# Kernel tuning notes

Hardware: AMD Instinct MI355X
Metric: run time of the kernel (lower is better)

## Reference

```python
import jax, jax.numpy as jnp
import numpy as np

N, D_FEAT, D, H, L = 2048, 128, 256, 8, 2
DH = D // H
E = 65536
NUM_EDGE_TYPES = 8
MAX_DIST = 10
MAX_DEGREE = 512
D_FF = 4 * D
D_OUT = 128
EPS = 1e-5


def _layernorm(x, g, b):
    mu = jnp.mean(x, axis=-1, keepdims=True)
    var = jnp.mean(jnp.square(x - mu), axis=-1, keepdims=True)
    return (x - mu) * jax.lax.rsqrt(var + EPS) * g + b


def setup_inputs() -> dict:
    key = jax.random.key(0)
    ks = jax.random.split(key, 32)
    inp = {
        "x": jax.random.normal(ks[0], (N, D_FEAT), dtype=jnp.float32),
        "edge_index": jax.random.randint(ks[1], (2, E), 0, N),
        "edge_types": jax.random.randint(ks[2], (E,), 0, NUM_EDGE_TYPES),
        "pos_encoding": jax.random.uniform(ks[3], (N, N), dtype=jnp.float32),
    }
    def xavier(k, shape):
        fan_in, fan_out = shape[0], shape[1]
        lim = float(np.sqrt(6.0 / (fan_in + fan_out)))
        return jax.random.uniform(k, shape, jnp.float32, -lim, lim)
    inp["W_emb"] = xavier(ks[4], (D_FEAT, D)); inp["b_emb"] = jnp.zeros((D,), jnp.float32)
    # stacked per-layer params, stored as [in, out] so y = x @ W + b
    inp["Wq"] = jnp.stack([xavier(jax.random.fold_in(ks[5], l), (D, D)) for l in range(L)])
    inp["Wk"] = jnp.stack([xavier(jax.random.fold_in(ks[6], l), (D, D)) for l in range(L)])
    inp["Wv"] = jnp.stack([xavier(jax.random.fold_in(ks[7], l), (D, D)) for l in range(L)])
    inp["Wo"] = jnp.stack([xavier(jax.random.fold_in(ks[8], l), (D, D)) for l in range(L)])
    for nm in ("bq", "bk", "bv", "bo"):
        inp[nm] = jnp.zeros((L, D), jnp.float32)
    inp["spd_table"] = 0.02 * jax.random.normal(ks[9], (L, MAX_DIST + 1, H), dtype=jnp.float32)
    inp["edge_table"] = 0.02 * jax.random.normal(ks[10], (L, NUM_EDGE_TYPES, H), dtype=jnp.float32)
    inp["din_emb"] = 0.02 * jax.random.normal(ks[11], (L, MAX_DEGREE + 1, D), dtype=jnp.float32)
    inp["dout_emb"] = 0.02 * jax.random.normal(ks[12], (L, MAX_DEGREE + 1, D), dtype=jnp.float32)
    inp["ln1_g"] = jnp.ones((L, D), jnp.float32); inp["ln1_b"] = jnp.zeros((L, D), jnp.float32)
    inp["ln2_g"] = jnp.ones((L, D), jnp.float32); inp["ln2_b"] = jnp.zeros((L, D), jnp.float32)
    inp["W1"] = jnp.stack([xavier(jax.random.fold_in(ks[13], l), (D, D_FF)) for l in range(L)])
    inp["b1"] = jnp.zeros((L, D_FF), jnp.float32)
    inp["W2"] = jnp.stack([xavier(jax.random.fold_in(ks[14], l), (D_FF, D)) for l in range(L)])
    inp["b2"] = jnp.zeros((L, D), jnp.float32)
    inp["W_out"] = xavier(ks[15], (D, D_OUT)); inp["b_out"] = jnp.zeros((D_OUT,), jnp.float32)
    return inp


def _forward(x, edge_index, edge_types, pos_encoding,
             W_emb, b_emb, Wq, bq, Wk, bk, Wv, bv, Wo, bo,
             spd_table, edge_table, din_emb, dout_emb,
             ln1_g, ln1_b, ln2_g, ln2_b, W1, b1, W2, b2, W_out, b_out):
    src, dst = edge_index[0], edge_index[1]
    ones = jnp.ones((E,), jnp.int32)
    deg_out = jnp.clip(jax.ops.segment_sum(ones, src, num_segments=N), 0, MAX_DEGREE)
    deg_in = jnp.clip(jax.ops.segment_sum(ones, dst, num_segments=N), 0, MAX_DEGREE)
    # SPD bucket matrix [N, N] (int), shared across layers
    spd_bucket = jnp.clip(pos_encoding[:, :N] * MAX_DIST + 0.5, 0, MAX_DIST).astype(jnp.int32)

    h = x @ W_emb + b_emb  # node embedding; dropout=0 (eval)
    scale = 1.0 / np.sqrt(DH)
    for l in range(L):
        # centrality encoding
        h = h + din_emb[l][deg_in] + dout_emb[l][deg_out]
        xn = _layernorm(h, ln1_g[l], ln1_b[l])
        q = (xn @ Wq[l] + bq[l]).reshape(N, H, DH).transpose(1, 0, 2)  # [H,N,DH]
        k = (xn @ Wk[l] + bk[l]).reshape(N, H, DH).transpose(1, 0, 2)
        v = (xn @ Wv[l] + bv[l]).reshape(N, H, DH).transpose(1, 0, 2)
        # attention bias [H, N, N]: SPD table gather + per-edge scatter-add
        bias = spd_table[l][spd_bucket].transpose(2, 0, 1)
        e_bias = edge_table[l][edge_types]  # [E, H]
        bias = bias.at[:, src, dst].add(e_bias.T)
        scores = jnp.einsum('hnd,hmd->hnm', q, k) * scale + bias
        attn = jax.nn.softmax(scores, axis=-1)
        attn_out = jnp.einsum('hnm,hmd->hnd', attn, v).transpose(1, 0, 2).reshape(N, D)
        h = h + attn_out @ Wo[l] + bo[l]
        y = _layernorm(h, ln2_g[l], ln2_b[l])
        y = jax.nn.gelu(y @ W1[l] + b1[l], approximate=False) @ W2[l] + b2[l]
        h = h + y
    return h @ W_out + b_out


def reference(x, edge_index, edge_types, pos_encoding,
              W_emb, b_emb, Wq, bq, Wk, bk, Wv, bv, Wo, bo,
              spd_table, edge_table, din_emb, dout_emb,
              ln1_g, ln1_b, ln2_g, ln2_b, W1, b1, W2, b2, W_out, b_out):
    return _forward(x, edge_index, edge_types, pos_encoding,
                    W_emb, b_emb, Wq, bq, Wk, bk, Wv, bv, Wo, bo,
                    spd_table, edge_table, din_emb, dout_emb,
                    ln1_g, ln1_b, ln2_g, ln2_b, W1, b1, W2, b2, W_out, b_out)
```

## Files before the change

### kernel.cpp

```cpp
#include <hip/hip_runtime.h>
#include <math.h>

#define N_NODES 2048
#define D_MODEL 256
#define D_FEAT 128
#define NHEAD 8
#define DH 32
#define NLAYER 2
#define NEDGE 65536
#define D_FF 1024
#define D_OUT 128
#define MAXDEG 512
#define JSPLIT 4

typedef __attribute__((ext_vector_type(8))) short short8;
typedef __attribute__((ext_vector_type(4))) float f32x4;
typedef __attribute__((ext_vector_type(4))) unsigned short u16x4;

__device__ __forceinline__ unsigned short f2bf(float f) {
    unsigned u = __float_as_uint(f);
    unsigned r = (u + 0x7FFFu + ((u >> 16) & 1u)) >> 16;
    return (unsigned short)r;
}

__global__ void degree_kernel(const int* __restrict__ edge_index,
                              int* __restrict__ deg_out, int* __restrict__ deg_in) {
    int e = blockIdx.x * 256 + threadIdx.x;
    if (e < NEDGE) {
        atomicAdd(&deg_out[edge_index[e]], 1);
        atomicAdd(&deg_in[edge_index[NEDGE + e]], 1);
    }
}

__global__ void centrality_kernel(float* __restrict__ h,
                                  const float* __restrict__ din_l,
                                  const float* __restrict__ dout_l,
                                  const int* __restrict__ deg_in,
                                  const int* __restrict__ deg_out) {
    int idx = blockIdx.x * 256 + threadIdx.x;
    int row = idx >> 8;
    int c = idx & 255;
    int di = min(deg_in[row], MAXDEG);
    int dn = min(deg_out[row], MAXDEG);
    h[idx] += din_l[di * D_MODEL + c] + dout_l[dn * D_MODEL + c];
}

__global__ void layernorm_kernel(const float* __restrict__ x,
                                 const float* __restrict__ g,
                                 const float* __restrict__ b,
                                 unsigned short* __restrict__ y) {
    int row = blockIdx.x;
    int tid = threadIdx.x;
    float v = x[row * D_MODEL + tid];
    __shared__ float red[256];
    red[tid] = v; __syncthreads();
    for (int s = 128; s > 0; s >>= 1) { if (tid < s) red[tid] += red[tid + s]; __syncthreads(); }
    float mu = red[0] * (1.0f / D_MODEL);
    __syncthreads();
    float d = v - mu;
    red[tid] = d * d; __syncthreads();
    for (int s = 128; s > 0; s >>= 1) { if (tid < s) red[tid] += red[tid + s]; __syncthreads(); }
    float rstd = rsqrtf(red[0] * (1.0f / D_MODEL) + 1e-5f);
    y[row * D_MODEL + tid] = f2bf(d * rstd * g[tid] + b[tid]);
}

__global__ void cast_kernel(const float* __restrict__ src, unsigned short* __restrict__ dst) {
    int i = blockIdx.x * 256 + threadIdx.x;
    float4 p = *(const float4*)&src[(size_t)i * 4];
    u16x4 o;
    o[0] = f2bf(p.x); o[1] = f2bf(p.y); o[2] = f2bf(p.z); o[3] = f2bf(p.w);
    *(u16x4*)&dst[(size_t)i * 4] = o;
}

__global__ void bucket_kernel(const float* __restrict__ pos, unsigned char* __restrict__ bucket) {
    int i = blockIdx.x * 256 + threadIdx.x;
    float4 p = *(const float4*)&pos[(size_t)i * 4];
    unsigned b0 = (unsigned)fminf(fmaxf(p.x * 10.f + 0.5f, 0.f), 10.f);
    unsigned b1 = (unsigned)fminf(fmaxf(p.y * 10.f + 0.5f, 0.f), 10.f);
    unsigned b2 = (unsigned)fminf(fmaxf(p.z * 10.f + 0.5f, 0.f), 10.f);
    unsigned b3 = (unsigned)fminf(fmaxf(p.w * 10.f + 0.5f, 0.f), 10.f);
    ((unsigned*)bucket)[i] = b0 | (b1 << 8) | (b2 << 16) | (b3 << 24);
}

__global__ void edge_hist_kernel(const int* __restrict__ ei, unsigned* __restrict__ hist) {
    int e = blockIdx.x * 256 + threadIdx.x;
    if (e < NEDGE) {
        int key = (ei[e] >> 6) * 2048 + ei[NEDGE + e];
        atomicAdd(&hist[key], 1);
    }
}

__global__ void edge_scan1_kernel(const unsigned* __restrict__ hist,
                                  unsigned* __restrict__ offsets, unsigned* __restrict__ blocksum) {
    __shared__ unsigned tmp[256];
    int t = threadIdx.x;
    int g = blockIdx.x * 256 + t;
    unsigned v = hist[g];
    tmp[t] = v; __syncthreads();
    for (int off = 1; off < 256; off <<= 1) {
        unsigned u = (t >= off) ? tmp[t - off] : 0;
        __syncthreads();
        tmp[t] += u;
        __syncthreads();
    }
    offsets[g] = tmp[t] - v;
    if (t == 255) blocksum[blockIdx.x] = tmp[255];
}

__global__ void edge_scan2_kernel(unsigned* __restrict__ blocksum) {
    __shared__ unsigned tmp[256];
    int t = threadIdx.x;
    unsigned v = blocksum[t];
    tmp[t] = v; __syncthreads();
    for (int off = 1; off < 256; off <<= 1) {
        unsigned u = (t >= off) ? tmp[t - off] : 0;
        __syncthreads();
        tmp[t] += u;
        __syncthreads();
    }
    blocksum[t] = tmp[t] - v;
}

__global__ void edge_scan3_kernel(const unsigned* __restrict__ blocksum,
                                  unsigned* __restrict__ offsets, unsigned* __restrict__ cursor) {
    int g = blockIdx.x * 256 + threadIdx.x;
    unsigned o = offsets[g] + blocksum[blockIdx.x];
    offsets[g] = o; cursor[g] = o;
    if (g == 0) offsets[65536] = NEDGE;
}

__global__ void edge_scatter_kernel(const int* __restrict__ ei, const int* __restrict__ etypes,
                                    unsigned* __restrict__ cursor, unsigned* __restrict__ packed) {
    int e = blockIdx.x * 256 + threadIdx.x;
    if (e < NEDGE) {
        int src = ei[e], dst = ei[NEDGE + e];
        int key = (src >> 6) * 2048 + dst;
        unsigned pos = atomicAdd(&cursor[key], 1);
        packed[pos] = (unsigned)dst | ((unsigned)(src & 63) << 11) | ((unsigned)etypes[e] << 17);
    }
}

__device__ __forceinline__ void wt_tile(const float* __restrict__ W, unsigned short* __restrict__ Wt,
                                        int K, int Nc, int n0, int k0, int tid,
                                        unsigned short (*tile)[33]) {
    int r = tid >> 3, cg = (tid & 7) * 4;
    float4 w4 = *(const float4*)&W[(size_t)(k0 + r) * Nc + n0 + cg];
    tile[r][cg + 0] = f2bf(w4.x); tile[r][cg + 1] = f2bf(w4.y);
    tile[r][cg + 2] = f2bf(w4.z); tile[r][cg + 3] = f2bf(w4.w);
    __syncthreads();
    int c = tid >> 3, rg = (tid & 7) * 4;
    u16x4 o;
    #pragma unroll
    for (int j = 0; j < 4; j++) o[j] = tile[rg + j][c];
    *(u16x4*)&Wt[(size_t)(n0 + c) * K + k0 + rg] = o;
}

__global__ void wt_qkvo_kernel(const float* __restrict__ Wq, const float* __restrict__ Wk,
                               const float* __restrict__ Wv, const float* __restrict__ Wo,
                               unsigned short* __restrict__ qkvt, unsigned short* __restrict__ wot) {
    __shared__ unsigned short tile[32][33];
    int z = blockIdx.z, l = z >> 2, which = z & 3;
    const float* W = (which == 0 ? Wq : which == 1 ? Wk : which == 2 ? Wv : Wo) + (size_t)l * 65536;
    unsigned short* dst = (which < 3) ? qkvt + (size_t)l * 196608 + which * 65536
                                      : wot + (size_t)l * 65536;
    wt_tile(W, dst, 256, 256, blockIdx.x * 32, blockIdx.y * 32, threadIdx.x, tile);
}

__global__ void wt_ffn1_kernel(const float* __restrict__ W1, unsigned short* __restrict__ w1t) {
    __shared__ unsigned short tile[32][33];
    int l = blockIdx.z;
    wt_tile(W1 + (size_t)l * D_MODEL * D_FF, w1t + (size_t)l * D_MODEL * D_FF,
            D_MODEL, D_FF, blockIdx.x * 32, blockIdx.y * 32, threadIdx.x, tile);
}

__global__ void wt_ffn2_kernel(const float* __restrict__ W2, unsigned short* __restrict__ w2t) {
    __shared__ unsigned short tile[32][33];
    int l = blockIdx.z;
    wt_tile(W2 + (size_t)l * D_FF * D_MODEL, w2t + (size_t)l * D_FF * D_MODEL,
            D_FF, D_MODEL, blockIdx.x * 32, blockIdx.y * 32, threadIdx.x, tile);
}

__global__ void wt_small_kernel(const float* __restrict__ W_emb, const float* __restrict__ W_out,
                                unsigned short* __restrict__ wembt, unsigned short* __restrict__ woutt) {
    __shared__ unsigned short tile[32][33];
    if (blockIdx.z == 0) {
        if (blockIdx.y >= 4) return;
        wt_tile(W_emb, wembt, D_FEAT, D_MODEL, blockIdx.x * 32, blockIdx.y * 32, threadIdx.x, tile);
    } else {
        if (blockIdx.x >= 4) return;
        wt_tile(W_out, woutt, D_MODEL, D_OUT, blockIdx.x * 32, blockIdx.y * 32, threadIdx.x, tile);
    }
}

__global__ void bias_stack_kernel(const float* __restrict__ bq, const float* __restrict__ bk,
                                  const float* __restrict__ bv, float* __restrict__ bqkv) {
    int i = blockIdx.x * 256 + threadIdx.x;
    int l = i / 768, j = i % 768;
    const float* src = j < 256 ? bq : j < 512 ? bk : bv;
    bqkv[i] = src[l * 256 + (j & 255)];
}

template <int ACT, bool RESID, bool OUTBF16>
__global__ void gemm_mfma_kernel(const unsigned short* __restrict__ A,
                                 const unsigned short* __restrict__ Wt,
                                 const float* __restrict__ bias,
                                 float* __restrict__ C, unsigned short* __restrict__ Cb,
                                 int Nc, int K) {
    __shared__ __align__(16) unsigned short As[32][72];
    __shared__ __align__(16) unsigned short Bs[64][72];
    int tid = threadIdx.x;
    int m0 = blockIdx.y * 32, n0 = blockIdx.x * 64;
    int w = tid >> 6, lane = tid & 63;
    int rg = (w & 1) * 16, cg = (w >> 1) * 32;
    int m = lane & 15, quad = lane >> 4;
    f32x4 acc[2] = {{0.f, 0.f, 0.f, 0.f}, {0.f, 0.f, 0.f, 0.f}};
    int ar = tid >> 3, ac = (tid & 7) * 8;
    for (int k0 = 0; k0 < K; k0 += 64) {
        *(uint4*)&As[ar][ac] = *(const uint4*)&A[(size_t)(m0 + ar) * K + k0 + ac];
        *(uint4*)&Bs[ar][ac] = *(const uint4*)&Wt[(size_t)(n0 + ar) * K + k0 + ac];
        *(uint4*)&Bs[ar + 32][ac] = *(const uint4*)&Wt[(size_t)(n0 + 32 + ar) * K + k0 + ac];
        __syncthreads();
        #pragma unroll
        for (int ks = 0; ks < 2; ks++) {
            short8 a = *(const short8*)&As[rg + m][ks * 32 + quad * 8];
            #pragma unroll
            for (int t = 0; t < 2; t++) {
                short8 b = *(const short8*)&Bs[cg + t * 16 + m][ks * 32 + quad * 8];
                acc[t] = __builtin_amdgcn_mfma_f32_16x16x32_bf16(a, b, acc[t], 0, 0, 0);
            }
        }
        __syncthreads();
    }
    #pragma unroll
    for (int t = 0; t < 2; t++) {
        #pragma unroll
        for (int reg = 0; reg < 4; reg++) {
            int row = m0 + rg + quad * 4 + reg;
            int col = n0 + cg + t * 16 + m;
            float val = acc[t][reg] + bias[col];
            if (ACT == 1) val = val * 0.5f * (1.0f + erff(val * 0.7071067811865476f));
            size_t idx = (size_t)row * Nc + col;
            if (RESID) val += C[idx];
            if (OUTBF16) Cb[idx] = f2bf(val);
            else C[idx] = val;
        }
    }
}

template <int ACT, bool OUTBF16>
__global__ void gemm64_kernel(const unsigned short* __restrict__ A,
                              const unsigned short* __restrict__ Wt,
                              const float* __restrict__ bias,
                              float* __restrict__ C, unsigned short* __restrict__ Cb,
                              int Nc, int K) {
    __shared__ __align__(16) unsigned short As[64][72];
    __shared__ __align__(16) unsigned short Bs[64][72];
    int tid = threadIdx.x;
    int m0 = blockIdx.y * 64, n0 = blockIdx.x * 64;
    int w = tid >> 6, lane = tid & 63;
    int wr = (w & 1) * 32, wc = (w >> 1) * 32;
    int m = lane & 15, quad = lane >> 4;
    f32x4 acc[2][2] = {{{0.f,0.f,0.f,0.f},{0.f,0.f,0.f,0.f}},{{0.f,0.f,0.f,0.f},{0.f,0.f,0.f,0.f}}};
    int sr = tid >> 2, sg = (tid & 3) * 16;
    for (int k0 = 0; k0 < K; k0 += 64) {
        *(uint4*)&As[sr][sg] = *(const uint4*)&A[(size_t)(m0 + sr) * K + k0 + sg];
        *(uint4*)&As[sr][sg + 8] = *(const uint4*)&A[(size_t)(m0 + sr) * K + k0 + sg + 8];
        *(uint4*)&Bs[sr][sg] = *(const uint4*)&Wt[(size_t)(n0 + sr) * K + k0 + sg];
        *(uint4*)&Bs[sr][sg + 8] = *(const uint4*)&Wt[(size_t)(n0 + sr) * K + k0 + sg + 8];
        __syncthreads();
        #pragma unroll
        for (int kh = 0; kh < 2; kh++) {
            short8 a0 = *(const short8*)&As[wr + m][kh * 32 + quad * 8];
            short8 a1 = *(const short8*)&As[wr + 16 + m][kh * 32 + quad * 8];
            short8 b0 = *(const short8*)&Bs[wc + m][kh * 32 + quad * 8];
            short8 b1 = *(const short8*)&Bs[wc + 16 + m][kh * 32 + quad * 8];
            acc[0][0] = __builtin_amdgcn_mfma_f32_16x16x32_bf16(a0, b0, acc[0][0], 0, 0, 0);
            acc[0][1] = __builtin_amdgcn_mfma_f32_16x16x32_bf16(a0, b1, acc[0][1], 0, 0, 0);
            acc[1][0] = __builtin_amdgcn_mfma_f32_16x16x32_bf16(a1, b0, acc[1][0], 0, 0, 0);
            acc[1][1] = __builtin_amdgcn_mfma_f32_16x16x32_bf16(a1, b1, acc[1][1], 0, 0, 0);
        }
        __syncthreads();
    }
    #pragma unroll
    for (int mt = 0; mt < 2; mt++) {
        #pragma unroll
        for (int nt = 0; nt < 2; nt++) {
            #pragma unroll
            for (int reg = 0; reg < 4; reg++) {
                int row = m0 + wr + mt * 16 + quad * 4 + reg;
                int col = n0 + wc + nt * 16 + m;
                float val = acc[mt][nt][reg] + bias[col];
                if (ACT == 1) val = val * 0.5f * (1.0f + erff(val * 0.7071067811865476f));
                size_t idx = (size_t)row * Nc + col;
                if (OUTBF16) Cb[idx] = f2bf(val);
                else C[idx] = val;
            }
        }
    }
}

__global__ void vbt_cast_kernel(const unsigned short* __restrict__ qkvb,
                                unsigned short* __restrict__ vbt) {
    __shared__ unsigned short tile[32][33];
    int c0 = blockIdx.x * 32, r0 = blockIdx.y * 32;
    int tid = threadIdx.x;
    int r = tid >> 3, cg = (tid & 7) * 4;
    u16x4 v4 = *(const u16x4*)&qkvb[(size_t)(r0 + r) * 768 + 512 + c0 + cg];
    tile[r][cg + 0] = v4[0]; tile[r][cg + 1] = v4[1];
    tile[r][cg + 2] = v4[2]; tile[r][cg + 3] = v4[3];
    __syncthreads();
    int c = tid >> 3, rg = (tid & 7) * 4;
    u16x4 o;
    #pragma unroll
    for (int j = 0; j < 4; j++) o[j] = tile[rg + j][c];
    *(u16x4*)&vbt[(size_t)(c0 + c) * N_NODES + r0 + rg] = o;
}

__global__ __launch_bounds__(256)
void flash_attn_kernel(const unsigned short* __restrict__ qkvb,
                       const unsigned short* __restrict__ vbt,
                       const unsigned char* __restrict__ bucket,
                       const float* __restrict__ spd_l,
                       const float* __restrict__ et_l,
                       const unsigned* __restrict__ offsets,
                       const unsigned* __restrict__ packed,
                       float* __restrict__ part_O,
                       float* __restrict__ m_part, float* __restrict__ l_part) {
    __shared__ __align__(16) unsigned short ks[64][40];
    __shared__ __align__(16) unsigned short vs[32][72];
    __shared__ __align__(16) float sbias[64][68];
    __shared__ __align__(16) unsigned short P[4][16][72];
    __shared__ float spd[11], et[8];

    int tid = threadIdx.x;
    int rb = blockIdx.x;
    int i0 = rb * 64;
    int hh = blockIdx.y;
    int js = blockIdx.z;
    if (tid < 11) spd[tid] = spd_l[tid * NHEAD + hh];
    else if (tid < 19) et[tid - 11] = et_l[(tid - 11) * NHEAD + hh];

    int w = tid >> 6, lane = tid & 63;
    int m = lane & 15, quad = lane >> 4;
    int r0 = w * 16;
    short8 aq = *(const short8*)&qkvb[(size_t)(i0 + r0 + m) * 768 + hh * DH + quad * 8];
    float m_st[4], l_st[4];
    #pragma unroll
    for (int r = 0; r < 4; r++) { m_st[r] = -3.0e38f; l_st[r] = 0.f; }
    f32x4 oacc[2] = {{0.f, 0.f, 0.f, 0.f}, {0.f, 0.f, 0.f, 0.f}};
    const float scale = 0.17677669529663687f;

    for (int jt = 0; jt < N_NODES / JSPLIT / 64; jt++) {
        int j0 = js * (N_NODES / JSPLIT) + jt * 64;
        __syncthreads();
        { int r = tid >> 2, kg = (tid & 3) * 8;
          *(uint4*)&ks[r][kg] = *(const uint4*)&qkvb[(size_t)(j0 + r) * 768 + 256 + hh * DH + kg]; }
        { int r = tid >> 3, cg = (tid & 7) * 8;
          *(uint4*)&vs[r][cg] = *(const uint4*)&vbt[(size_t)(hh * DH + r) * N_NODES + j0 + cg]; }
        { int r = tid >> 2, cg = (tid & 3) * 16;
          uint4 b16 = *(const uint4*)&bucket[(size_t)(i0 + r) * N_NODES + j0 + cg];
          const unsigned char* bb = (const unsigned char*)&b16;
          #pragma unroll
          for (int i = 0; i < 16; i++) sbias[r][cg + i] = spd[bb[i]];
        }
        __syncthreads();
        { unsigned key0 = (unsigned)rb * 2048 + j0;
          unsigned start = offsets[key0], end = offsets[key0 + 64];
          for (unsigned i = start + tid; i < end; i += 256) {
              unsigned p = packed[i];
              atomicAdd(&sbias[(p >> 11) & 63][(p & 2047) - j0], et[(p >> 17) & 7]);
          }
        }
        __syncthreads();
        float sv[4][4];
        #pragma unroll
        for (int t = 0; t < 4; t++) {
            short8 bk8 = *(const short8*)&ks[t * 16 + m][quad * 8];
            f32x4 z = {0.f, 0.f, 0.f, 0.f};
            f32x4 sacc = __builtin_amdgcn_mfma_f32_16x16x32_bf16(aq, bk8, z, 0, 0, 0);
            #pragma unroll
            for (int r = 0; r < 4; r++)
                sv[t][r] = sacc[r] * scale + sbias[r0 + quad * 4 + r][t * 16 + m];
        }
        float alpha[4];
        #pragma unroll
        for (int r = 0; r < 4; r++) {
            float mx = fmaxf(fmaxf(sv[0][r], sv[1][r]), fmaxf(sv[2][r], sv[3][r]));
            #pragma unroll
            for (int off = 1; off < 16; off <<= 1) mx = fmaxf(mx, __shfl_xor(mx, off, 64));
            float mn = fmaxf(m_st[r], mx);
            alpha[r] = __expf(m_st[r] - mn);
            m_st[r] = mn;
            float ps = 0.f;
            #pragma unroll
            for (int t = 0; t < 4; t++) { float pv = __expf(sv[t][r] - mn); sv[t][r] = pv; ps += pv; }
            #pragma unroll
            for (int off = 1; off < 16; off <<= 1) ps += __shfl_xor(ps, off, 64);
            l_st[r] = l_st[r] * alpha[r] + ps;
        }
        #pragma unroll
        for (int t = 0; t < 4; t++)
            #pragma unroll
            for (int r = 0; r < 4; r++)
                P[w][quad * 4 + r][t * 16 + m] = f2bf(sv[t][r]);
        #pragma unroll
        for (int r = 0; r < 4; r++) { oacc[0][r] *= alpha[r]; oacc[1][r] *= alpha[r]; }
        __builtin_amdgcn_s_waitcnt(0xC07F);
        #pragma unroll
        for (int kh = 0; kh < 2; kh++) {
            short8 pa = *(const short8*)&P[w][m][kh * 32 + quad * 8];
            #pragma unroll
            for (int t = 0; t < 2; t++) {
                short8 vb = *(const short8*)&vs[t * 16 + m][kh * 32 + quad * 8];
                oacc[t] = __builtin_amdgcn_mfma_f32_16x16x32_bf16(pa, vb, oacc[t], 0, 0, 0);
            }
        }
    }
    #pragma unroll
    for (int t = 0; t < 2; t++)
        #pragma unroll
        for (int r = 0; r < 4; r++)
            part_O[((size_t)js * N_NODES + i0 + r0 + quad * 4 + r) * D_MODEL + hh * DH + t * 16 + m] =
                oacc[t][r];
    if (m == 0) {
        #pragma unroll
        for (int r = 0; r < 4; r++) {
            int row = i0 + r0 + quad * 4 + r;
            m_part[((size_t)js * NHEAD + hh) * N_NODES + row] = m_st[r];
            l_part[((size_t)js * NHEAD + hh) * N_NODES + row] = l_st[r];
        }
    }
}

__global__ void flash_merge_kernel(const float* __restrict__ part_O,
                                   const float* __restrict__ m_part,
                                   const float* __restrict__ l_part,
                                   unsigned short* __restrict__ aoutb) {
    int e = blockIdx.x * 256 + threadIdx.x;
    int row = e >> 8, col = e & 255, h = col >> 5;
    float mv[JSPLIT];
    float mg = -3.0e38f;
    #pragma unroll
    for (int js = 0; js < JSPLIT; js++) {
        mv[js] = m_part[((size_t)js * NHEAD + h) * N_NODES + row];
        mg = fmaxf(mg, mv[js]);
    }
    float o = 0.f, l = 0.f;
    #pragma unroll
    for (int js = 0; js < JSPLIT; js++) {
        float sc = __expf(mv[js] - mg);
        o += sc * part_O[(size_t)js * N_NODES * D_MODEL + e];
        l += sc * l_part[((size_t)js * NHEAD + h) * N_NODES + row];
    }
    aoutb[e] = f2bf(o / l);
}

extern "C" void kernel_launch(void* const* d_in, const int* in_sizes, int n_in,
                              void* d_out, int out_size, void* d_ws, size_t ws_size,
                              hipStream_t stream) {
    const float* x          = (const float*)d_in[0];
    const int*   edge_index = (const int*)d_in[1];
    const int*   edge_types = (const int*)d_in[2];
    const float* pos        = (const float*)d_in[3];
    const float* W_emb      = (const float*)d_in[4];
    const float* b_emb      = (const float*)d_in[5];
    const float* Wq         = (const float*)d_in[6];
    const float* Wk         = (const float*)d_in[7];
    const float* Wv         = (const float*)d_in[8];
    const float* Wo         = (const float*)d_in[9];
    const float* bq         = (const float*)d_in[10];
    const float* bk         = (const float*)d_in[11];
    const float* bv         = (const float*)d_in[12];
    const float* bo         = (const float*)d_in[13];
    const float* spd_table  = (const float*)d_in[14];
    const float* edge_table = (const float*)d_in[15];
    const float* din_emb    = (const float*)d_in[16];
    const float* dout_emb   = (const float*)d_in[17];
    const float* ln1_g      = (const float*)d_in[18];
    const float* ln1_b      = (const float*)d_in[19];
    const float* ln2_g      = (const float*)d_in[20];
    const float* ln2_b      = (const float*)d_in[21];
    const float* W1         = (const float*)d_in[22];
    const float* b1         = (const float*)d_in[23];
    const float* W2         = (const float*)d_in[24];
    const float* b2         = (const float*)d_in[25];
    const float* W_out      = (const float*)d_in[26];
    const float* b_out      = (const float*)d_in[27];
    float* out = (float*)d_out;

    char* base = (char*)d_ws;
    int* deg_out = (int*)base;                    base += (size_t)N_NODES * 4;
    int* deg_in  = (int*)base;                    base += (size_t)N_NODES * 4;
    float* h     = (float*)base;                  base += (size_t)N_NODES * D_MODEL * 4;
    unsigned short* hb   = (unsigned short*)base; base += (size_t)N_NODES * D_MODEL * 2;
    unsigned short* xb   = (unsigned short*)base; base += (size_t)N_NODES * D_MODEL * 2;
    unsigned short* xb0  = (unsigned short*)base; base += (size_t)N_NODES * D_FEAT * 2;
    unsigned short* qkvb = (unsigned short*)base; base += (size_t)N_NODES * 768 * 2;
    unsigned short* vbt  = (unsigned short*)base; base += (size_t)D_MODEL * N_NODES * 2;
    unsigned short* aoutb = (unsigned short*)base; base += (size_t)N_NODES * D_MODEL * 2;
    unsigned short* ffnb = (unsigned short*)base; base += (size_t)N_NODES * D_FF * 2;
    unsigned char* bucket = (unsigned char*)base; base += (size_t)N_NODES * N_NODES;
    unsigned short* qkvt = (unsigned short*)base; base += (size_t)NLAYER * 768 * D_MODEL * 2;
    unsigned short* wot  = (unsigned short*)base; base += (size_t)NLAYER * D_MODEL * D_MODEL * 2;
    unsigned short* w1t  = (unsigned short*)base; base += (size_t)NLAYER * D_MODEL * D_FF * 2;
    unsigned short* w2t  = (unsigned short*)base; base += (size_t)NLAYER * D_FF * D_MODEL * 2;
    unsigned short* wembt = (unsigned short*)base; base += (size_t)D_FEAT * D_MODEL * 2;
    unsigned short* woutt = (unsigned short*)base; base += (size_t)D_MODEL * D_OUT * 2;
    float* bqkv = (float*)base;                   base += (size_t)NLAYER * 768 * 4;
    unsigned* hist    = (unsigned*)base;          base += (size_t)65536 * 4;
    unsigned* offsets = (unsigned*)base;          base += (size_t)65537 * 4;
    unsigned* cursor  = (unsigned*)base;          base += (size_t)65536 * 4;
    unsigned* blocksum = (unsigned*)base;         base += (size_t)256 * 4;
    unsigned* packed  = (unsigned*)base;          base += (size_t)NEDGE * 4;
    float* part_O = (float*)base;                 base += (size_t)JSPLIT * N_NODES * D_MODEL * 4;
    float* m_part = (float*)base;                 base += (size_t)JSPLIT * NHEAD * N_NODES * 4;
    float* l_part = (float*)base;                 base += (size_t)JSPLIT * NHEAD * N_NODES * 4;

    hipMemsetAsync(deg_out, 0, (size_t)N_NODES * 4 * 2, stream);
    hipMemsetAsync(hist, 0, (size_t)65536 * 4, stream);

    degree_kernel<<<NEDGE / 256, 256, 0, stream>>>(edge_index, deg_out, deg_in);

    edge_hist_kernel<<<NEDGE / 256, 256, 0, stream>>>(edge_index, hist);
    edge_scan1_kernel<<<256, 256, 0, stream>>>(hist, offsets, blocksum);
    edge_scan2_kernel<<<1, 256, 0, stream>>>(blocksum);
    edge_scan3_kernel<<<256, 256, 0, stream>>>(blocksum, offsets, cursor);
    edge_scatter_kernel<<<NEDGE / 256, 256, 0, stream>>>(edge_index, edge_types, cursor, packed);
    wt_qkvo_kernel<<<dim3(8, 8, NLAYER * 4), 256, 0, stream>>>(Wq, Wk, Wv, Wo, qkvt, wot);
    wt_ffn1_kernel<<<dim3(D_FF / 32, D_MODEL / 32, NLAYER), 256, 0, stream>>>(W1, w1t);
    wt_ffn2_kernel<<<dim3(D_MODEL / 32, D_FF / 32, NLAYER), 256, 0, stream>>>(W2, w2t);
    wt_small_kernel<<<dim3(8, 8, 2), 256, 0, stream>>>(W_emb, W_out, wembt, woutt);
    bias_stack_kernel<<<NLAYER * 768 / 256, 256, 0, stream>>>(bq, bk, bv, bqkv);
    bucket_kernel<<<(size_t)N_NODES * N_NODES / 4 / 256, 256, 0, stream>>>(pos, bucket);
    cast_kernel<<<N_NODES * D_FEAT / 4 / 256, 256, 0, stream>>>(x, xb0);

    gemm_mfma_kernel<0, false, false><<<dim3(D_MODEL / 64, N_NODES / 32), 256, 0, stream>>>(
        xb0, wembt, b_emb, h, nullptr, D_MODEL, D_FEAT);

    for (int l = 0; l < NLAYER; l++) {
        centrality_kernel<<<N_NODES * D_MODEL / 256, 256, 0, stream>>>(
            h, din_emb + (size_t)l * (MAXDEG + 1) * D_MODEL,
            dout_emb + (size_t)l * (MAXDEG + 1) * D_MODEL, deg_in, deg_out);

        layernorm_kernel<<<N_NODES, 256, 0, stream>>>(h, ln1_g + l * D_MODEL, ln1_b + l * D_MODEL, xb);

        gemm64_kernel<0, true><<<dim3(768 / 64, N_NODES / 64), 256, 0, stream>>>(
            xb, qkvt + (size_t)l * 768 * D_MODEL, bqkv + l * 768, nullptr, qkvb, 768, D_MODEL);

        vbt_cast_kernel<<<dim3(D_MODEL / 32, N_NODES / 32), 256, 0, stream>>>(qkvb, vbt);

        flash_attn_kernel<<<dim3(N_NODES / 64, NHEAD, JSPLIT), 256, 0, stream>>>(
            qkvb, vbt, bucket, spd_table + (size_t)l * 11 * NHEAD,
            edge_table + (size_t)l * 8 * NHEAD, offsets, packed, part_O, m_part, l_part);

        flash_merge_kernel<<<N_NODES * D_MODEL / 256, 256, 0, stream>>>(part_O, m_part, l_part, aoutb);

        gemm_mfma_kernel<0, true, false><<<dim3(D_MODEL / 64, N_NODES / 32), 256, 0, stream>>>(
            aoutb, wot + (size_t)l * D_MODEL * D_MODEL, bo + l * D_MODEL, h, nullptr, D_MODEL, D_MODEL);

        layernorm_kernel<<<N_NODES, 256, 0, stream>>>(h, ln2_g + l * D_MODEL, ln2_b + l * D_MODEL, xb);

        gemm64_kernel<1, true><<<dim3(D_FF / 64, N_NODES / 64), 256, 0, stream>>>(
            xb, w1t + (size_t)l * D_MODEL * D_FF, b1 + l * D_FF, nullptr, ffnb, D_FF, D_MODEL);

        gemm_mfma_kernel<0, true, false><<<dim3(D_MODEL / 64, N_NODES / 32), 256, 0, stream>>>(
            ffnb, w2t + (size_t)l * D_FF * D_MODEL, b2 + l * D_MODEL, h, nullptr, D_MODEL, D_FF);
    }

    cast_kernel<<<N_NODES * D_MODEL / 4 / 256, 256, 0, stream>>>(h, hb);
    gemm_mfma_kernel<0, false, false><<<dim3(D_OUT / 64, N_NODES / 32), 256, 0, stream>>>(
        hb, woutt, b_out, out, nullptr, D_OUT, D_MODEL);
}
```

Baseline: 349.7 us.

## Fuse preprocessing, casts, centrality+LN, V transpose and rework attention bias path

Merges the degree and histogram kernels, the weight-transpose and bias-stack kernels, and centrality with layernorm into single launches. The fp32-to-bf16 casts move into the GEMM A-load, and the V transpose moves into the QKV GEMM epilogue. The GEMM gains register prefetch of the next K tile, and the attention kernel switches its row reductions to DPP ops and reuses one fp32 LDS tile for both bias and P. These cuts aim at launch overhead and extra global round trips, in exchange for more LDS traffic and fp32 P storage in attention.

Result: faster. 314.4 us (-10.1%).

```diff
diff --git a/kernel.cpp b/kernel.cpp
--- a/kernel.cpp
+++ b/kernel.cpp
@@ -23,26 +23,107 @@
     return (unsigned short)r;
 }
 
-__global__ void degree_kernel(const int* __restrict__ edge_index,
-                              int* __restrict__ deg_out, int* __restrict__ deg_in) {
+template <int CTRL>
+__device__ __forceinline__ float dpp_ror(float x) {
+    return __int_as_float(__builtin_amdgcn_update_dpp(0, __float_as_int(x), CTRL, 0xf, 0xf, false));
+}
+
+__global__ void degree_hist_kernel(const int* __restrict__ ei,
+                                   int* __restrict__ deg_out, int* __restrict__ deg_in,
+                                   unsigned* __restrict__ hist) {
     int e = blockIdx.x * 256 + threadIdx.x;
     if (e < NEDGE) {
-        atomicAdd(&deg_out[edge_index[e]], 1);
-        atomicAdd(&deg_in[edge_index[NEDGE + e]], 1);
-    }
-}
-
-__global__ void centrality_kernel(float* __restrict__ h,
-                                  const float* __restrict__ din_l,
-                                  const float* __restrict__ dout_l,
-                                  const int* __restrict__ deg_in,
-                                  const int* __restrict__ deg_out) {
-    int idx = blockIdx.x * 256 + threadIdx.x;
-    int row = idx >> 8;
-    int c = idx & 255;
+        int src = ei[e], dst = ei[NEDGE + e];
+        atomicAdd(&deg_out[src], 1);
+        atomicAdd(&deg_in[dst], 1);
+        atomicAdd(&hist[(src >> 6) * 2048 + dst], 1);
+    }
+}
+
+__global__ void edge_scan1_kernel(const unsigned* __restrict__ hist,
+                                  unsigned* __restrict__ offsets, unsigned* __restrict__ blocksum) {
+    __shared__ unsigned tmp[256];
+    int t = threadIdx.x;
+    int g = blockIdx.x * 256 + t;
+    unsigned v = hist[g];
+    tmp[t] = v; __syncthreads();
+    for (int off = 1; off < 256; off <<= 1) {
+        unsigned u = (t >= off) ? tmp[t - off] : 0;
+        __syncthreads();
+        tmp[t] += u;
+        __syncthreads();
+    }
+    offsets[g] = tmp[t] - v;
+    if (t == 255) blocksum[blockIdx.x] = tmp[255];
+}
+
+__global__ void edge_scan2_kernel(unsigned* __restrict__ blocksum) {
+    __shared__ unsigned tmp[256];
+    int t = threadIdx.x;
+    unsigned v = blocksum[t];
+    tmp[t] = v; __syncthreads();
+    for (int off = 1; off < 256; off <<= 1) {
+        unsigned u = (t >= off) ? tmp[t - off] : 0;
+        __syncthreads();
+        tmp[t] += u;
+        __syncthreads();
+    }
+    blocksum[t] = tmp[t] - v;
+}
+
+__global__ void edge_scan3_kernel(const unsigned* __restrict__ blocksum,
+                                  unsigned* __restrict__ offsets, unsigned* __restrict__ cursor) {
+    int g = blockIdx.x * 256 + threadIdx.x;
+    unsigned o = offsets[g] + blocksum[blockIdx.x];
+    offsets[g] = o; cursor[g] = o;
+    if (g == 0) offsets[65536] = NEDGE;
+}
+
+__global__ void edge_scatter_kernel(const int* __restrict__ ei, const int* __restrict__ etypes,
+                                    unsigned* __restrict__ cursor, unsigned* __restrict__ packed) {
+    int e = blockIdx.x * 256 + threadIdx.x;
+    if (e < NEDGE) {
+        int src = ei[e], dst = ei[NEDGE + e];
+        int key = (src >> 6) * 2048 + dst;
+        unsigned pos = atomicAdd(&cursor[key], 1);
+        packed[pos] = (unsigned)dst | ((unsigned)(src & 63) << 11) | ((unsigned)etypes[e] << 17);
+    }
+}
+
+__global__ void bucket_kernel(const float* __restrict__ pos, unsigned char* __restrict__ bucket) {
+    int i = blockIdx.x * 256 + threadIdx.x;
+    float4 p = *(const float4*)&pos[(size_t)i * 4];
+    unsigned b0 = (unsigned)fminf(fmaxf(p.x * 10.f + 0.5f, 0.f), 10.f);
+    unsigned b1 = (unsigned)fminf(fmaxf(p.y * 10.f + 0.5f, 0.f), 10.f);
+    unsigned b2 = (unsigned)fminf(fmaxf(p.z * 10.f + 0.5f, 0.f), 10.f);
+    unsigned b3 = (unsigned)fminf(fmaxf(p.w * 10.f + 0.5f, 0.f), 10.f);
+    ((unsigned*)bucket)[i] = b0 | (b1 << 8) | (b2 << 16) | (b3 << 24);
+}
+
+__global__ void centrality_ln_kernel(float* __restrict__ h,
+                                     const float* __restrict__ din_l,
+                                     const float* __restrict__ dout_l,
+                                     const int* __restrict__ deg_in,
+                                     const int* __restrict__ deg_out,
+                                     const float* __restrict__ g,
+                                     const float* __restrict__ b,
+                                     unsigned short* __restrict__ y) {
+    int row = blockIdx.x;
+    int tid = threadIdx.x;
     int di = min(deg_in[row], MAXDEG);
     int dn = min(deg_out[row], MAXDEG);
-    h[idx] += din_l[di * D_MODEL + c] + dout_l[dn * D_MODEL + c];
+    float v = h[row * D_MODEL + tid] + din_l[di * D_MODEL + tid] + dout_l[dn * D_MODEL + tid];
+    h[row * D_MODEL + tid] = v;
+    __shared__ float red[256];
+    red[tid] = v; __syncthreads();
+    for (int s = 128; s > 0; s >>= 1) { if (tid < s) red[tid] += red[tid + s]; __syncthreads(); }
+    float mu = red[0] * (1.0f / D_MODEL);
+    __syncthreads();
+    float d = v - mu;
+    red[tid] = d * d; __syncthreads();
+    for (int s = 128; s > 0; s >>= 1) { if (tid < s) red[tid] += red[tid + s]; __syncthreads(); }
+    float rstd = rsqrtf(red[0] * (1.0f / D_MODEL) + 1e-5f);
+    y[row * D_MODEL + tid] = f2bf(d * rstd * g[tid] + b[tid]);
 }
 
 __global__ void layernorm_kernel(const float* __restrict__ x,
@@ -64,82 +145,6 @@
     y[row * D_MODEL + tid] = f2bf(d * rstd * g[tid] + b[tid]);
 }
 
-__global__ void cast_kernel(const float* __restrict__ src, unsigned short* __restrict__ dst) {
-    int i = blockIdx.x * 256 + threadIdx.x;
-    float4 p = *(const float4*)&src[(size_t)i * 4];
-    u16x4 o;
-    o[0] = f2bf(p.x); o[1] = f2bf(p.y); o[2] = f2bf(p.z); o[3] = f2bf(p.w);
-    *(u16x4*)&dst[(size_t)i * 4] = o;
-}
-
-__global__ void bucket_kernel(const float* __restrict__ pos, unsigned char* __restrict__ bucket) {
-    int i = blockIdx.x * 256 + threadIdx.x;
-    float4 p = *(const float4*)&pos[(size_t)i * 4];
-    unsigned b0 = (unsigned)fminf(fmaxf(p.x * 10.f + 0.5f, 0.f), 10.f);
-    unsigned b1 = (unsigned)fminf(fmaxf(p.y * 10.f + 0.5f, 0.f), 10.f);
-    unsigned b2 = (unsigned)fminf(fmaxf(p.z * 10.f + 0.5f, 0.f), 10.f);
-    unsigned b3 = (unsigned)fminf(fmaxf(p.w * 10.f + 0.5f, 0.f), 10.f);
-    ((unsigned*)bucket)[i] = b0 | (b1 << 8) | (b2 << 16) | (b3 << 24);
-}
-
-__global__ void edge_hist_kernel(const int* __restrict__ ei, unsigned* __restrict__ hist) {
-    int e = blockIdx.x * 256 + threadIdx.x;
-    if (e < NEDGE) {
-        int key = (ei[e] >> 6) * 2048 + ei[NEDGE + e];
-        atomicAdd(&hist[key], 1);
-    }
-}
-
-__global__ void edge_scan1_kernel(const unsigned* __restrict__ hist,
-                                  unsigned* __restrict__ offsets, unsigned* __restrict__ blocksum) {
-    __shared__ unsigned tmp[256];
-    int t = threadIdx.x;
-    int g = blockIdx.x * 256 + t;
-    unsigned v = hist[g];
-    tmp[t] = v; __syncthreads();
-    for (int off = 1; off < 256; off <<= 1) {
-        unsigned u = (t >= off) ? tmp[t - off] : 0;
-        __syncthreads();
-        tmp[t] += u;
-        __syncthreads();
-    }
-    offsets[g] = tmp[t] - v;
-    if (t == 255) blocksum[blockIdx.x] = tmp[255];
-}
-
-__global__ void edge_scan2_kernel(unsigned* __restrict__ blocksum) {
-    __shared__ unsigned tmp[256];
-    int t = threadIdx.x;
-    unsigned v = blocksum[t];
-    tmp[t] = v; __syncthreads();
-    for (int off = 1; off < 256; off <<= 1) {
-        unsigned u = (t >= off) ? tmp[t - off] : 0;
-        __syncthreads();
-        tmp[t] += u;
-        __syncthreads();
-    }
-    blocksum[t] = tmp[t] - v;
-}
-
-__global__ void edge_scan3_kernel(const unsigned* __restrict__ blocksum,
-                                  unsigned* __restrict__ offsets, unsigned* __restrict__ cursor) {
-    int g = blockIdx.x * 256 + threadIdx.x;
-    unsigned o = offsets[g] + blocksum[blockIdx.x];
-    offsets[g] = o; cursor[g] = o;
-    if (g == 0) offsets[65536] = NEDGE;
-}
-
-__global__ void edge_scatter_kernel(const int* __restrict__ ei, const int* __restrict__ etypes,
-                                    unsigned* __restrict__ cursor, unsigned* __restrict__ packed) {
-    int e = blockIdx.x * 256 + threadIdx.x;
-    if (e < NEDGE) {
-        int src = ei[e], dst = ei[NEDGE + e];
-        int key = (src >> 6) * 2048 + dst;
-        unsigned pos = atomicAdd(&cursor[key], 1);
-        packed[pos] = (unsigned)dst | ((unsigned)(src & 63) << 11) | ((unsigned)etypes[e] << 17);
-    }
-}
-
 __device__ __forceinline__ void wt_tile(const float* __restrict__ W, unsigned short* __restrict__ Wt,
                                         int K, int Nc, int n0, int k0, int tid,
                                         unsigned short (*tile)[33]) {
@@ -155,59 +160,59 @@
     *(u16x4*)&Wt[(size_t)(n0 + c) * K + k0 + rg] = o;
 }
 
-__global__ void wt_qkvo_kernel(const float* __restrict__ Wq, const float* __restrict__ Wk,
-                               const float* __restrict__ Wv, const float* __restrict__ Wo,
-                               unsigned short* __restrict__ qkvt, unsigned short* __restrict__ wot) {
+__global__ void wt_all_kernel(const float* __restrict__ Wq, const float* __restrict__ Wk,
+                              const float* __restrict__ Wv, const float* __restrict__ Wo,
+                              const float* __restrict__ W1, const float* __restrict__ W2,
+                              const float* __restrict__ W_emb, const float* __restrict__ W_out,
+                              const float* __restrict__ bq, const float* __restrict__ bk,
+                              const float* __restrict__ bv,
+                              unsigned short* __restrict__ qkvt, unsigned short* __restrict__ wot,
+                              unsigned short* __restrict__ w1t, unsigned short* __restrict__ w2t,
+                              unsigned short* __restrict__ wembt, unsigned short* __restrict__ woutt,
+                              float* __restrict__ bqkv) {
     __shared__ unsigned short tile[32][33];
-    int z = blockIdx.z, l = z >> 2, which = z & 3;
-    const float* W = (which == 0 ? Wq : which == 1 ? Wk : which == 2 ? Wv : Wo) + (size_t)l * 65536;
-    unsigned short* dst = (which < 3) ? qkvt + (size_t)l * 196608 + which * 65536
-                                      : wot + (size_t)l * 65536;
-    wt_tile(W, dst, 256, 256, blockIdx.x * 32, blockIdx.y * 32, threadIdx.x, tile);
-}
-
-__global__ void wt_ffn1_kernel(const float* __restrict__ W1, unsigned short* __restrict__ w1t) {
-    __shared__ unsigned short tile[32][33];
-    int l = blockIdx.z;
-    wt_tile(W1 + (size_t)l * D_MODEL * D_FF, w1t + (size_t)l * D_MODEL * D_FF,
-            D_MODEL, D_FF, blockIdx.x * 32, blockIdx.y * 32, threadIdx.x, tile);
-}
-
-__global__ void wt_ffn2_kernel(const float* __restrict__ W2, unsigned short* __restrict__ w2t) {
-    __shared__ unsigned short tile[32][33];
-    int l = blockIdx.z;
-    wt_tile(W2 + (size_t)l * D_FF * D_MODEL, w2t + (size_t)l * D_FF * D_MODEL,
-            D_FF, D_MODEL, blockIdx.x * 32, blockIdx.y * 32, threadIdx.x, tile);
-}
-
-__global__ void wt_small_kernel(const float* __restrict__ W_emb, const float* __restrict__ W_out,
-                                unsigned short* __restrict__ wembt, unsigned short* __restrict__ woutt) {
-    __shared__ unsigned short tile[32][33];
-    if (blockIdx.z == 0) {
-        if (blockIdx.y >= 4) return;
-        wt_tile(W_emb, wembt, D_FEAT, D_MODEL, blockIdx.x * 32, blockIdx.y * 32, threadIdx.x, tile);
+    int b = blockIdx.x, tid = threadIdx.x;
+    if (b < 512) {
+        int z = b >> 6, t = b & 63;
+        int l = z >> 2, which = z & 3;
+        const float* W = (which == 0 ? Wq : which == 1 ? Wk : which == 2 ? Wv : Wo) + (size_t)l * 65536;
+        unsigned short* dst = (which < 3) ? qkvt + (size_t)l * 196608 + which * 65536
+                                          : wot + (size_t)l * 65536;
+        wt_tile(W, dst, 256, 256, (t & 7) * 32, (t >> 3) * 32, tid, tile);
+    } else if (b < 1024) {
+        int b2 = b - 512, l = b2 >> 8, t = b2 & 255;
+        wt_tile(W1 + (size_t)l * D_MODEL * D_FF, w1t + (size_t)l * D_MODEL * D_FF,
+                D_MODEL, D_FF, (t & 31) * 32, (t >> 5) * 32, tid, tile);
+    } else if (b < 1536) {
+        int b3 = b - 1024, l = b3 >> 8, t = b3 & 255;
+        wt_tile(W2 + (size_t)l * D_FF * D_MODEL, w2t + (size_t)l * D_FF * D_MODEL,
+                D_FF, D_MODEL, (t & 7) * 32, (t >> 3) * 32, tid, tile);
+    } else if (b < 1568) {
+        int b4 = b - 1536;
+        wt_tile(W_emb, wembt, D_FEAT, D_MODEL, (b4 & 7) * 32, (b4 >> 3) * 32, tid, tile);
+    } else if (b < 1600) {
+        int b5 = b - 1568;
+        wt_tile(W_out, woutt, D_MODEL, D_OUT, (b5 & 3) * 32, (b5 >> 2) * 32, tid, tile);
     } else {
-        if (blockIdx.x >= 4) return;
-        wt_tile(W_out, woutt, D_MODEL, D_OUT, blockIdx.x * 32, blockIdx.y * 32, threadIdx.x, tile);
-    }
-}
-
-__global__ void bias_stack_kernel(const float* __restrict__ bq, const float* __restrict__ bk,
-                                  const float* __restrict__ bv, float* __restrict__ bqkv) {
-    int i = blockIdx.x * 256 + threadIdx.x;
-    int l = i / 768, j = i % 768;
-    const float* src = j < 256 ? bq : j < 512 ? bk : bv;
-    bqkv[i] = src[l * 256 + (j & 255)];
-}
-
-template <int ACT, bool RESID, bool OUTBF16>
-__global__ void gemm_mfma_kernel(const unsigned short* __restrict__ A,
+        int i = (b - 1600) * 256 + tid;
+        if (i < NLAYER * 768) {
+            int l = i / 768, j = i % 768;
+            const float* src = j < 256 ? bq : j < 512 ? bk : bv;
+            bqkv[i] = src[l * 256 + (j & 255)];
+        }
+    }
+}
+
+template <int ACT, bool RESID, bool OUTBF16, bool AFP32>
+__global__ void gemm_mfma_kernel(const void* __restrict__ Av,
                                  const unsigned short* __restrict__ Wt,
                                  const float* __restrict__ bias,
                                  float* __restrict__ C, unsigned short* __restrict__ Cb,
                                  int Nc, int K) {
     __shared__ __align__(16) unsigned short As[32][72];
     __shared__ __align__(16) unsigned short Bs[64][72];
+    const unsigned short* A16 = (const unsigned short*)Av;
+    const float* A32 = (const float*)Av;
     int tid = threadIdx.x;
     int m0 = blockIdx.y * 32, n0 = blockIdx.x * 64;
     int w = tid >> 6, lane = tid & 63;
@@ -215,11 +220,38 @@
     int m = lane & 15, quad = lane >> 4;
     f32x4 acc[2] = {{0.f, 0.f, 0.f, 0.f}, {0.f, 0.f, 0.f, 0.f}};
     int ar = tid >> 3, ac = (tid & 7) * 8;
+    uint4 ra; float4 fa0, fa1; uint4 rb0, rb1;
+    if (AFP32) {
+        fa0 = *(const float4*)&A32[(size_t)(m0 + ar) * K + ac];
+        fa1 = *(const float4*)&A32[(size_t)(m0 + ar) * K + ac + 4];
+    } else {
+        ra = *(const uint4*)&A16[(size_t)(m0 + ar) * K + ac];
+    }
+    rb0 = *(const uint4*)&Wt[(size_t)(n0 + ar) * K + ac];
+    rb1 = *(const uint4*)&Wt[(size_t)(n0 + 32 + ar) * K + ac];
     for (int k0 = 0; k0 < K; k0 += 64) {
-        *(uint4*)&As[ar][ac] = *(const uint4*)&A[(size_t)(m0 + ar) * K + k0 + ac];
-        *(uint4*)&Bs[ar][ac] = *(const uint4*)&Wt[(size_t)(n0 + ar) * K + k0 + ac];
-        *(uint4*)&Bs[ar + 32][ac] = *(const uint4*)&Wt[(size_t)(n0 + 32 + ar) * K + k0 + ac];
-        __syncthreads();
+        if (AFP32) {
+            u16x4 t0 = {f2bf(fa0.x), f2bf(fa0.y), f2bf(fa0.z), f2bf(fa0.w)};
+            u16x4 t1 = {f2bf(fa1.x), f2bf(fa1.y), f2bf(fa1.z), f2bf(fa1.w)};
+            *(u16x4*)&As[ar][ac] = t0;
+            *(u16x4*)&As[ar][ac + 4] = t1;
+        } else {
+            *(uint4*)&As[ar][ac] = ra;
+        }
+        *(uint4*)&Bs[ar][ac] = rb0;
+        *(uint4*)&Bs[ar + 32][ac] = rb1;
+        __syncthreads();
+        int kn = k0 + 64;
+        if (kn < K) {
+            if (AFP32) {
+                fa0 = *(const float4*)&A32[(size_t)(m0 + ar) * K + kn + ac];
+                fa1 = *(const float4*)&A32[(size_t)(m0 + ar) * K + kn + ac + 4];
+            } else {
+                ra = *(const uint4*)&A16[(size_t)(m0 + ar) * K + kn + ac];
+            }
+            rb0 = *(const uint4*)&Wt[(size_t)(n0 + ar) * K + kn + ac];
+            rb1 = *(const uint4*)&Wt[(size_t)(n0 + 32 + ar) * K + kn + ac];
+        }
         #pragma unroll
         for (int ks = 0; ks < 2; ks++) {
             short8 a = *(const short8*)&As[rg + m][ks * 32 + quad * 8];
@@ -247,11 +279,12 @@
     }
 }
 
-template <int ACT, bool OUTBF16>
+template <int ACT, bool VBT>
 __global__ void gemm64_kernel(const unsigned short* __restrict__ A,
                               const unsigned short* __restrict__ Wt,
                               const float* __restrict__ bias,
-                              float* __restrict__ C, unsigned short* __restrict__ Cb,
+                              unsigned short* __restrict__ Cb,
+                              unsigned short* __restrict__ vbt,
                               int Nc, int K) {
     __shared__ __align__(16) unsigned short As[64][72];
     __shared__ __align__(16) unsigned short Bs[64][72];
@@ -262,22 +295,33 @@
     int m = lane & 15, quad = lane >> 4;
     f32x4 acc[2][2] = {{{0.f,0.f,0.f,0.f},{0.f,0.f,0.f,0.f}},{{0.f,0.f,0.f,0.f},{0.f,0.f,0.f,0.f}}};
     int sr = tid >> 2, sg = (tid & 3) * 16;
+    uint4 a0 = *(const uint4*)&A[(size_t)(m0 + sr) * K + sg];
+    uint4 a1 = *(const uint4*)&A[(size_t)(m0 + sr) * K + sg + 8];
+    uint4 b0 = *(const uint4*)&Wt[(size_t)(n0 + sr) * K + sg];
+    uint4 b1 = *(const uint4*)&Wt[(size_t)(n0 + sr) * K + sg + 8];
     for (int k0 = 0; k0 < K; k0 += 64) {
-        *(uint4*)&As[sr][sg] = *(const uint4*)&A[(size_t)(m0 + sr) * K + k0 + sg];
-        *(uint4*)&As[sr][sg + 8] = *(const uint4*)&A[(size_t)(m0 + sr) * K + k0 + sg + 8];
-        *(uint4*)&Bs[sr][sg] = *(const uint4*)&Wt[(size_t)(n0 + sr) * K + k0 + sg];
-        *(uint4*)&Bs[sr][sg + 8] = *(const uint4*)&Wt[(size_t)(n0 + sr) * K + k0 + sg + 8];
-        __syncthreads();
+        *(uint4*)&As[sr][sg] = a0;
+        *(uint4*)&As[sr][sg + 8] = a1;
+        *(uint4*)&Bs[sr][sg] = b0;
+        *(uint4*)&Bs[sr][sg + 8] = b1;
+        __syncthreads();
+        int kn = k0 + 64;
+        if (kn < K) {
+            a0 = *(const uint4*)&A[(size_t)(m0 + sr) * K + kn + sg];
+            a1 = *(const uint4*)&A[(size_t)(m0 + sr) * K + kn + sg + 8];
+            b0 = *(const uint4*)&Wt[(size_t)(n0 + sr) * K + kn + sg];
+            b1 = *(const uint4*)&Wt[(size_t)(n0 + sr) * K + kn + sg + 8];
+        }
         #pragma unroll
         for (int kh = 0; kh < 2; kh++) {
-            short8 a0 = *(const short8*)&As[wr + m][kh * 32 + quad * 8];
-            short8 a1 = *(const short8*)&As[wr + 16 + m][kh * 32 + quad * 8];
-            short8 b0 = *(const short8*)&Bs[wc + m][kh * 32 + quad * 8];
-            short8 b1 = *(const short8*)&Bs[wc + 16 + m][kh * 32 + quad * 8];
-            acc[0][0] = __builtin_amdgcn_mfma_f32_16x16x32_bf16(a0, b0, acc[0][0], 0, 0, 0);
-            acc[0][1] = __builtin_amdgcn_mfma_f32_16x16x32_bf16(a0, b1, acc[0][1], 0, 0, 0);
-            acc[1][0] = __builtin_amdgcn_mfma_f32_16x16x32_bf16(a1, b0, acc[1][0], 0, 0, 0);
-            acc[1][1] = __builtin_amdgcn_mfma_f32_16x16x32_bf16(a1, b1, acc[1][1], 0, 0, 0);
+            short8 x0 = *(const short8*)&As[wr + m][kh * 32 + quad * 8];
+            short8 x1 = *(const short8*)&As[wr + 16 + m][kh * 32 + quad * 8];
+            short8 y0 = *(const short8*)&Bs[wc + m][kh * 32 + quad * 8];
+            short8 y1 = *(const short8*)&Bs[wc + 16 + m][kh * 32 + quad * 8];
+            acc[0][0] = __builtin_amdgcn_mfma_f32_16x16x32_bf16(x0, y0, acc[0][0], 0, 0, 0);
+            acc[0][1] = __builtin_amdgcn_mfma_f32_16x16x32_bf16(x0, y1, acc[0][1], 0, 0, 0);
+            acc[1][0] = __builtin_amdgcn_mfma_f32_16x16x32_bf16(x1, y0, acc[1][0], 0, 0, 0);
+            acc[1][1] = __builtin_amdgcn_mfma_f32_16x16x32_bf16(x1, y1, acc[1][1], 0, 0, 0);
         }
         __syncthreads();
     }
@@ -291,29 +335,13 @@
                 int col = n0 + wc + nt * 16 + m;
                 float val = acc[mt][nt][reg] + bias[col];
                 if (ACT == 1) val = val * 0.5f * (1.0f + erff(val * 0.7071067811865476f));
-                size_t idx = (size_t)row * Nc + col;
-                if (OUTBF16) Cb[idx] = f2bf(val);
-                else C[idx] = val;
+                unsigned short bv = f2bf(val);
+                Cb[(size_t)row * Nc + col] = bv;
+                if (VBT && col >= 512)
+                    vbt[(size_t)(col - 512) * N_NODES + row] = bv;
             }
         }
     }
-}
-
-__global__ void vbt_cast_kernel(const unsigned short* __restrict__ qkvb,
-                                unsigned short* __restrict__ vbt) {
-    __shared__ unsigned short tile[32][33];
-    int c0 = blockIdx.x * 32, r0 = blockIdx.y * 32;
-    int tid = threadIdx.x;
-    int r = tid >> 3, cg = (tid & 7) * 4;
-    u16x4 v4 = *(const u16x4*)&qkvb[(size_t)(r0 + r) * 768 + 512 + c0 + cg];
-    tile[r][cg + 0] = v4[0]; tile[r][cg + 1] = v4[1];
-    tile[r][cg + 2] = v4[2]; tile[r][cg + 3] = v4[3];
-    __syncthreads();
-    int c = tid >> 3, rg = (tid & 7) * 4;
-    u16x4 o;
-    #pragma unroll
-    for (int j = 0; j < 4; j++) o[j] = tile[rg + j][c];
-    *(u16x4*)&vbt[(size_t)(c0 + c) * N_NODES + r0 + rg] = o;
 }
 
 __global__ __launch_bounds__(256)
@@ -328,19 +356,19 @@
                        float* __restrict__ m_part, float* __restrict__ l_part) {
     __shared__ __align__(16) unsigned short ks[64][40];
     __shared__ __align__(16) unsigned short vs[32][72];
-    __shared__ __align__(16) float sbias[64][68];
-    __shared__ __align__(16) unsigned short P[4][16][72];
-    __shared__ float spd[11], et[8];
+    __shared__ __align__(16) float ov[64][68];
+    __shared__ float et[8];
 
     int tid = threadIdx.x;
     int rb = blockIdx.x;
     int i0 = rb * 64;
     int hh = blockIdx.y;
     int js = blockIdx.z;
-    if (tid < 11) spd[tid] = spd_l[tid * NHEAD + hh];
-    else if (tid < 19) et[tid - 11] = et_l[(tid - 11) * NHEAD + hh];
-
-    int w = tid >> 6, lane = tid & 63;
+    int lane = tid & 63;
+    if (tid < 8) et[tid] = et_l[tid * NHEAD + hh];
+    float spd_reg = spd_l[(lane < 11 ? lane : 10) * NHEAD + hh];
+
+    int w = tid >> 6;
     int m = lane & 15, quad = lane >> 4;
     int r0 = w * 16;
     short8 aq = *(const short8*)&qkvb[(size_t)(i0 + r0 + m) * 768 + hh * DH + quad * 8];
@@ -350,26 +378,39 @@
     f32x4 oacc[2] = {{0.f, 0.f, 0.f, 0.f}, {0.f, 0.f, 0.f, 0.f}};
     const float scale = 0.17677669529663687f;
 
+    int krow = tid >> 2, kcol = (tid & 3) * 8;
+    int vrow = tid >> 3, vcol = (tid & 7) * 8;
+    int brow = tid >> 2, bcol = (tid & 3) * 16;
+
     for (int jt = 0; jt < N_NODES / JSPLIT / 64; jt++) {
         int j0 = js * (N_NODES / JSPLIT) + jt * 64;
         __syncthreads();
-        { int r = tid >> 2, kg = (tid & 3) * 8;
-          *(uint4*)&ks[r][kg] = *(const uint4*)&qkvb[(size_t)(j0 + r) * 768 + 256 + hh * DH + kg]; }
-        { int r = tid >> 3, cg = (tid & 7) * 8;
-          *(uint4*)&vs[r][cg] = *(const uint4*)&vbt[(size_t)(hh * DH + r) * N_NODES + j0 + cg]; }
-        { int r = tid >> 2, cg = (tid & 3) * 16;
-          uint4 b16 = *(const uint4*)&bucket[(size_t)(i0 + r) * N_NODES + j0 + cg];
-          const unsigned char* bb = (const unsigned char*)&b16;
-          #pragma unroll
-          for (int i = 0; i < 16; i++) sbias[r][cg + i] = spd[bb[i]];
-        }
-        __syncthreads();
-        { unsigned key0 = (unsigned)rb * 2048 + j0;
-          unsigned start = offsets[key0], end = offsets[key0 + 64];
-          for (unsigned i = start + tid; i < end; i += 256) {
-              unsigned p = packed[i];
-              atomicAdd(&sbias[(p >> 11) & 63][(p & 2047) - j0], et[(p >> 17) & 7]);
-          }
+        *(uint4*)&ks[krow][kcol] =
+            *(const uint4*)&qkvb[(size_t)(j0 + krow) * 768 + 256 + hh * DH + kcol];
+        *(uint4*)&vs[vrow][vcol] =
+            *(const uint4*)&vbt[(size_t)(hh * DH + vrow) * N_NODES + j0 + vcol];
+        {
+            uint4 b16 = *(const uint4*)&bucket[(size_t)(i0 + brow) * N_NODES + j0 + bcol];
+            const unsigned char* bb = (const unsigned char*)&b16;
+            float fb[16];
+            #pragma unroll
+            for (int i = 0; i < 16; i++)
+                fb[i] = __int_as_float(
+                    __builtin_amdgcn_ds_bpermute(((int)bb[i]) << 2, __float_as_int(spd_reg)));
+            #pragma unroll
+            for (int g = 0; g < 4; g++) {
+                f32x4 st = {fb[g * 4], fb[g * 4 + 1], fb[g * 4 + 2], fb[g * 4 + 3]};
+                *(f32x4*)&ov[brow][bcol + g * 4] = st;
+            }
+        }
+        __syncthreads();
+        {
+            unsigned key0 = (unsigned)rb * 2048 + j0;
+            unsigned start = offsets[key0], end = offsets[key0 + 64];
+            for (unsigned i = start + tid; i < end; i += 256) {
+                unsigned p = packed[i];
+                atomicAdd(&ov[(p >> 11) & 63][(p & 2047) - j0], et[(p >> 17) & 7]);
+            }
         }
         __syncthreads();
         float sv[4][4];
@@ -380,35 +421,45 @@
             f32x4 sacc = __builtin_amdgcn_mfma_f32_16x16x32_bf16(aq, bk8, z, 0, 0, 0);
             #pragma unroll
             for (int r = 0; r < 4; r++)
-                sv[t][r] = sacc[r] * scale + sbias[r0 + quad * 4 + r][t * 16 + m];
+                sv[t][r] = sacc[r] * scale + ov[r0 + quad * 4 + r][t * 16 + m];
         }
         float alpha[4];
         #pragma unroll
         for (int r = 0; r < 4; r++) {
             float mx = fmaxf(fmaxf(sv[0][r], sv[1][r]), fmaxf(sv[2][r], sv[3][r]));
-            #pragma unroll
-            for (int off = 1; off < 16; off <<= 1) mx = fmaxf(mx, __shfl_xor(mx, off, 64));
+            mx = fmaxf(mx, dpp_ror<0x121>(mx));
+            mx = fmaxf(mx, dpp_ror<0x122>(mx));
+            mx = fmaxf(mx, dpp_ror<0x124>(mx));
+            mx = fmaxf(mx, dpp_ror<0x128>(mx));
             float mn = fmaxf(m_st[r], mx);
             alpha[r] = __expf(m_st[r] - mn);
             m_st[r] = mn;
             float ps = 0.f;
             #pragma unroll
             for (int t = 0; t < 4; t++) { float pv = __expf(sv[t][r] - mn); sv[t][r] = pv; ps += pv; }
-            #pragma unroll
-            for (int off = 1; off < 16; off <<= 1) ps += __shfl_xor(ps, off, 64);
+            ps += dpp_ror<0x121>(ps);
+            ps += dpp_ror<0x122>(ps);
+            ps += dpp_ror<0x124>(ps);
+            ps += dpp_ror<0x128>(ps);
             l_st[r] = l_st[r] * alpha[r] + ps;
         }
         #pragma unroll
         for (int t = 0; t < 4; t++)
             #pragma unroll
             for (int r = 0; r < 4; r++)
-                P[w][quad * 4 + r][t * 16 + m] = f2bf(sv[t][r]);
+                ov[r0 + quad * 4 + r][t * 16 + m] = sv[t][r];
         #pragma unroll
         for (int r = 0; r < 4; r++) { oacc[0][r] *= alpha[r]; oacc[1][r] *= alpha[r]; }
         __builtin_amdgcn_s_waitcnt(0xC07F);
         #pragma unroll
         for (int kh = 0; kh < 2; kh++) {
-            short8 pa = *(const short8*)&P[w][m][kh * 32 + quad * 8];
+            f32x4 p0 = *(const f32x4*)&ov[r0 + m][kh * 32 + quad * 8];
+            f32x4 p1 = *(const f32x4*)&ov[r0 + m][kh * 32 + quad * 8 + 4];
+            short8 pa;
+            pa[0] = (short)f2bf(p0[0]); pa[1] = (short)f2bf(p0[1]);
+            pa[2] = (short)f2bf(p0[2]); pa[3] = (short)f2bf(p0[3]);
+            pa[4] = (short)f2bf(p1[0]); pa[5] = (short)f2bf(p1[1]);
+            pa[6] = (short)f2bf(p1[2]); pa[7] = (short)f2bf(p1[3]);
             #pragma unroll
             for (int t = 0; t < 2; t++) {
                 short8 vb = *(const short8*)&vs[t * 16 + m][kh * 32 + quad * 8];
@@ -492,9 +543,7 @@
     int* deg_out = (int*)base;                    base += (size_t)N_NODES * 4;
     int* deg_in  = (int*)base;                    base += (size_t)N_NODES * 4;
     float* h     = (float*)base;                  base += (size_t)N_NODES * D_MODEL * 4;
-    unsigned short* hb   = (unsigned short*)base; base += (size_t)N_NODES * D_MODEL * 2;
     unsigned short* xb   = (unsigned short*)base; base += (size_t)N_NODES * D_MODEL * 2;
-    unsigned short* xb0  = (unsigned short*)base; base += (size_t)N_NODES * D_FEAT * 2;
     unsigned short* qkvb = (unsigned short*)base; base += (size_t)N_NODES * 768 * 2;
     unsigned short* vbt  = (unsigned short*)base; base += (size_t)D_MODEL * N_NODES * 2;
     unsigned short* aoutb = (unsigned short*)base; base += (size_t)N_NODES * D_MODEL * 2;
@@ -519,35 +568,26 @@
     hipMemsetAsync(deg_out, 0, (size_t)N_NODES * 4 * 2, stream);
     hipMemsetAsync(hist, 0, (size_t)65536 * 4, stream);
 
-    degree_kernel<<<NEDGE / 256, 256, 0, stream>>>(edge_index, deg_out, deg_in);
-
-    edge_hist_kernel<<<NEDGE / 256, 256, 0, stream>>>(edge_index, hist);
+    degree_hist_kernel<<<NEDGE / 256, 256, 0, stream>>>(edge_index, deg_out, deg_in, hist);
     edge_scan1_kernel<<<256, 256, 0, stream>>>(hist, offsets, blocksum);
     edge_scan2_kernel<<<1, 256, 0, stream>>>(blocksum);
     edge_scan3_kernel<<<256, 256, 0, stream>>>(blocksum, offsets, cursor);
     edge_scatter_kernel<<<NEDGE / 256, 256, 0, stream>>>(edge_index, edge_types, cursor, packed);
-    wt_qkvo_kernel<<<dim3(8, 8, NLAYER * 4), 256, 0, stream>>>(Wq, Wk, Wv, Wo, qkvt, wot);
-    wt_ffn1_kernel<<<dim3(D_FF / 32, D_MODEL / 32, NLAYER), 256, 0, stream>>>(W1, w1t);
-    wt_ffn2_kernel<<<dim3(D_MODEL / 32, D_FF / 32, NLAYER), 256, 0, stream>>>(W2, w2t);
-    wt_small_kernel<<<dim3(8, 8, 2), 256, 0, stream>>>(W_emb, W_out, wembt, woutt);
-    bias_stack_kernel<<<NLAYER * 768 / 256, 256, 0, stream>>>(bq, bk, bv, bqkv);
+    wt_all_kernel<<<1606, 256, 0, stream>>>(Wq, Wk, Wv, Wo, W1, W2, W_emb, W_out,
+                                            bq, bk, bv, qkvt, wot, w1t, w2t, wembt, woutt, bqkv);
     bucket_kernel<<<(size_t)N_NODES * N_NODES / 4 / 256, 256, 0, stream>>>(pos, bucket);
-    cast_kernel<<<N_NODES * D_FEAT / 4 / 256, 256, 0, stream>>>(x, xb0);
-
-    gemm_mfma_kernel<0, false, false><<<dim3(D_MODEL / 64, N_NODES / 32), 256, 0, stream>>>(
-        xb0, wembt, b_emb, h, nullptr, D_MODEL, D_FEAT);
+
+    gemm_mfma_kernel<0, false, false, true><<<dim3(D_MODEL / 64, N_NODES / 32), 256, 0, stream>>>(
+        x, wembt, b_emb, h, nullptr, D_MODEL, D_FEAT);
 
     for (int l = 0; l < NLAYER; l++) {
-        centrality_kernel<<<N_NODES * D_MODEL / 256, 256, 0, stream>>>(
+        centrality_ln_kernel<<<N_NODES, 256, 0, stream>>>(
             h, din_emb + (size_t)l * (MAXDEG + 1) * D_MODEL,
-            dout_emb + (size_t)l * (MAXDEG + 1) * D_MODEL, deg_in, deg_out);
-
-        layernorm_kernel<<<N_NODES, 256, 0, stream>>>(h, ln1_g + l * D_MODEL, ln1_b + l * D_MODEL, xb);
+            dout_emb + (size_t)l * (MAXDEG + 1) * D_MODEL, deg_in, deg_out,
+            ln1_g + l * D_MODEL, ln1_b + l * D_MODEL, xb);
 
         gemm64_kernel<0, true><<<dim3(768 / 64, N_NODES / 64), 256, 0, stream>>>(
-            xb, qkvt + (size_t)l * 768 * D_MODEL, bqkv + l * 768, nullptr, qkvb, 768, D_MODEL);
-
-        vbt_cast_kernel<<<dim3(D_MODEL / 32, N_NODES / 32), 256, 0, stream>>>(qkvb, vbt);
+            xb, qkvt + (size_t)l * 768 * D_MODEL, bqkv + l * 768, qkvb, vbt, 768, D_MODEL);
 
         flash_attn_kernel<<<dim3(N_NODES / 64, NHEAD, JSPLIT), 256, 0, stream>>>(
             qkvb, vbt, bucket, spd_table + (size_t)l * 11 * NHEAD,
@@ -555,19 +595,18 @@
 
         flash_merge_kernel<<<N_NODES * D_MODEL / 256, 256, 0, stream>>>(part_O, m_part, l_part, aoutb);
 
-        gemm_mfma_kernel<0, true, false><<<dim3(D_MODEL / 64, N_NODES / 32), 256, 0, stream>>>(
+        gemm_mfma_kernel<0, true, false, false><<<dim3(D_MODEL / 64, N_NODES / 32), 256, 0, stream>>>(
             aoutb, wot + (size_t)l * D_MODEL * D_MODEL, bo + l * D_MODEL, h, nullptr, D_MODEL, D_MODEL);
 
         layernorm_kernel<<<N_NODES, 256, 0, stream>>>(h, ln2_g + l * D_MODEL, ln2_b + l * D_MODEL, xb);
 
-        gemm64_kernel<1, true><<<dim3(D_FF / 64, N_NODES / 64), 256, 0, stream>>>(
-            xb, w1t + (size_t)l * D_MODEL * D_FF, b1 + l * D_FF, nullptr, ffnb, D_FF, D_MODEL);
-
-        gemm_mfma_kernel<0, true, false><<<dim3(D_MODEL / 64, N_NODES / 32), 256, 0, stream>>>(
+        gemm64_kernel<1, false><<<dim3(D_FF / 64, N_NODES / 64), 256, 0, stream>>>(
+            xb, w1t + (size_t)l * D_MODEL * D_FF, b1 + l * D_FF, ffnb, nullptr, D_FF, D_MODEL);
+
+        gemm_mfma_kernel<0, true, false, false><<<dim3(D_MODEL / 64, N_NODES / 32), 256, 0, stream>>>(
             ffnb, w2t + (size_t)l * D_FF * D_MODEL, b2 + l * D_MODEL, h, nullptr, D_MODEL, D_FF);
     }
 
-    cast_kernel<<<N_NODES * D_MODEL / 4 / 256, 256, 0, stream>>>(h, hb);
-    gemm_mfma_kernel<0, false, false><<<dim3(D_OUT / 64, N_NODES / 32), 256, 0, stream>>>(
-        hb, woutt, b_out, out, nullptr, D_OUT, D_MODEL);
-}
+    gemm_mfma_kernel<0, false, false, true><<<dim3(D_OUT / 64, N_NODES / 32), 256, 0, stream>>>(
+        h, woutt, b_out, out, nullptr, D_OUT, D_MODEL);
+}
```
